# Kernel tuning notes

Measured on AMD Instinct MI355X. Metric: run time of the kernel, lower is better.

Reference implementation:

```python
import jax, jax.numpy as jnp
import numpy as np

N = 100000
E = 1600000
IN_DIM = 256
HID = 128


def setup_inputs() -> dict:
    key = jax.random.key(0)
    k = jax.random.split(key, 8)
    x = jax.random.normal(k[0], (N, IN_DIM), dtype=jnp.float32)
    edge_index = jax.random.randint(k[1], (2, E), 0, N, dtype=jnp.int64 if jax.config.jax_enable_x64 else jnp.int32)
    # GCNConv weight (no bias pre-aggregation; bias added after aggregation, as in PyG)
    W_conv = jax.random.normal(k[2], (IN_DIM, HID), dtype=jnp.float32) / np.sqrt(IN_DIM)
    b_conv = jnp.zeros((HID,), dtype=jnp.float32)
    prelu_a = jnp.full((1,), 0.25, dtype=jnp.float32)  # torch.nn.PReLU default init
    W_lin = jax.random.normal(k[3], (HID, IN_DIM), dtype=jnp.float32) / np.sqrt(HID)
    b_lin = jnp.zeros((IN_DIM,), dtype=jnp.float32)
    return {"x": x, "edge_index": edge_index, "W_conv": W_conv, "b_conv": b_conv,
            "prelu_a": prelu_a, "W_lin": W_lin, "b_lin": b_lin}


def _gcn_conv(x, edge_index, W, b):
    # h = x @ W  ([N, HID])
    h = x @ W
    src, dst = edge_index[0], edge_index[1]
    # add self-loops
    loops = jnp.arange(N, dtype=src.dtype)
    src = jnp.concatenate([src, loops])
    dst = jnp.concatenate([dst, loops])
    # symmetric degree normalization deg^-1/2 (degree over incoming edges incl. self-loops)
    deg = jax.ops.segment_sum(jnp.ones_like(dst, dtype=h.dtype), dst, num_segments=N)
    dinv = jnp.where(deg > 0, jax.lax.rsqrt(deg), 0.0)
    norm = dinv[src] * dinv[dst]                     # [E+N]
    msg = h[src] * norm[:, None]                     # gather + scale  [E+N, HID]
    out = jax.ops.segment_sum(msg, dst, num_segments=N)  # scatter-add  [N, HID]
    return out + b


def reference(x, edge_index, W_conv, b_conv, prelu_a, W_lin, b_lin):
    h = _gcn_conv(x, edge_index, W_conv, b_conv)
    h = jnp.where(h >= 0, h, prelu_a * h)            # PReLU (single shared slope)
    # dropout p=0.0 -> identity
    return h @ W_lin + b_lin                          # [N, IN_DIM]
```

## Files before the change

kernel.cpp:

```cpp
#include <hip/hip_runtime.h>

#define N_NODES 100000
#define E_EDGES 1600000
#define INDIM 256
#define HID 128
#define CAP 48
#define NPART 8
#define PART_SZ 12500
#define ECAP 32768
#define PA_BLOCKS 1563
#define PA_STRIDE (PA_BLOCKS * 256)
#define G1_BLOCKS 1563
#define PB_BLOCKS 1024
#define GG_BLOCKS 3125

typedef __attribute__((ext_vector_type(8))) short s16x8;
typedef __attribute__((ext_vector_type(4))) float f32x4;
typedef __attribute__((ext_vector_type(4))) unsigned int u32x4;

__device__ __forceinline__ unsigned short cvt_bf16(float f) {
    unsigned int u = __float_as_uint(f);
    u += 0x7FFFu + ((u >> 16) & 1u);
    return (unsigned short)(u >> 16);
}
__device__ __forceinline__ float bf16_to_f(unsigned short s) {
    return __uint_as_float(((unsigned int)s) << 16);
}

__global__ __launch_bounds__(256) void parta_kernel(const int* __restrict__ src,
                                                    const int* __restrict__ dst,
                                                    int* __restrict__ gcnt,
                                                    unsigned int* __restrict__ pedges,
                                                    const float* __restrict__ Wc,
                                                    const float* __restrict__ Wl,
                                                    unsigned short* __restrict__ f1,
                                                    unsigned short* __restrict__ f2,
                                                    int* __restrict__ count) {
    __shared__ int sCount[8];
    __shared__ int sBase[8];
    const int tid = threadIdx.x;

    if (blockIdx.x < 256) {
        int pt = blockIdx.x * 256 + tid;
        if (pt < 32768) {
            int j = pt & 7, L = (pt >> 3) & 63, t = (pt >> 9) & 7, c = pt >> 12;
            int k = c * 32 + ((L >> 4) * 8) + j;
            int n = t * 16 + (L & 15);
            f1[pt] = cvt_bf16(Wc[k * 128 + n]);
        } else {
            int u = pt - 32768;
            int j = u & 7, L = (u >> 3) & 63, t = (u >> 9) & 15, c = u >> 13;
            int k = c * 32 + ((L >> 4) * 8) + j;
            int n = t * 16 + (L & 15);
            f2[u] = cvt_bf16(Wl[k * 256 + n]);
        }
    } else if (blockIdx.x < 512) {
        for (int i = (blockIdx.x - 256) * 256 + tid; i < 100000; i += 256 * 256)
            count[i] = 0;
    }

    if (tid < 8) sCount[tid] = 0;
    __syncthreads();
    const int lane = tid & 63;
    const int t0 = blockIdx.x * 256 + tid;
    const int xcd = blockIdx.x & 7;

    unsigned int pk[4];
    int pp[4];
    int lo[4];
#pragma unroll
    for (int r = 0; r < 4; ++r) {
        int e = t0 + r * PA_STRIDE;
        bool valid = e < E_EDGES;
        int d = 0, s = 0;
        if (valid) {
            d = __builtin_nontemporal_load(dst + e);
            s = __builtin_nontemporal_load(src + e);
        }
        int p = valid ? d / PART_SZ : 8;
        unsigned long long mask_p = 0ull;
#pragma unroll
        for (int v = 0; v < 8; ++v) {
            unsigned long long mv = __ballot(p == v);
            if (p == v) mask_p = mv;
        }
        int off = __popcll(mask_p & ((1ull << lane) - 1ull));
        int ldr = (mask_p == 0ull) ? 0 : (__ffsll(mask_p) - 1);
        int wbase = 0;
        if (valid && lane == ldr) wbase = atomicAdd(&sCount[p], __popcll(mask_p));
        wbase = __shfl(wbase, ldr);
        pp[r] = p;
        lo[r] = wbase + off;
        pk[r] = ((unsigned int)(d - p * PART_SZ) << 17) | (unsigned int)s;
    }
    __syncthreads();
    if (tid < 8) sBase[tid] = atomicAdd(&gcnt[xcd * 8 + tid], sCount[tid]);
    __syncthreads();
#pragma unroll
    for (int r = 0; r < 4; ++r) {
        if (pp[r] < 8) {
            int pos = sBase[pp[r]] + lo[r];
            if (pos < ECAP)
                __builtin_nontemporal_store(pk[r],
                    pedges + (size_t)(xcd * 8 + pp[r]) * ECAP + pos);
        }
    }
}

__global__ __launch_bounds__(256) void fat_kernel(const float* __restrict__ x,
                                                  const unsigned short* __restrict__ fragW,
                                                  unsigned short* __restrict__ h,
                                                  const unsigned int* __restrict__ pedges,
                                                  const int* __restrict__ gcnt,
                                                  int* __restrict__ count,
                                                  int* __restrict__ bucket) {
    __shared__ __align__(16) unsigned short xs[64 * 48];
    const int tid = threadIdx.x;

    if (blockIdx.x < G1_BLOCKS) {
        const int r0 = blockIdx.x * 64;
        const int w = tid >> 6, lane = tid & 63;
        const int q = lane >> 4, m = lane & 15;
        const int srow = tid >> 2, skg = tid & 3;

        f32x4 acc[8];
#pragma unroll
        for (int t = 0; t < 8; ++t) acc[t] = (f32x4){0.f, 0.f, 0.f, 0.f};

        const s16x8* fwv = (const s16x8*)fragW;

        for (int c = 0; c < 8; ++c) {
            int gr = r0 + srow;
            f32x4 v0 = (f32x4){0.f, 0.f, 0.f, 0.f}, v1 = v0;
            if (gr < N_NODES) {
                const f32x4* p = (const f32x4*)&x[(size_t)gr * INDIM + c * 32 + skg * 8];
                v0 = __builtin_nontemporal_load(p);
                v1 = __builtin_nontemporal_load(p + 1);
            }
            uint4 pk;
            pk.x = ((unsigned)cvt_bf16(v0.y) << 16) | cvt_bf16(v0.x);
            pk.y = ((unsigned)cvt_bf16(v0.w) << 16) | cvt_bf16(v0.z);
            pk.z = ((unsigned)cvt_bf16(v1.y) << 16) | cvt_bf16(v1.x);
            pk.w = ((unsigned)cvt_bf16(v1.w) << 16) | cvt_bf16(v1.z);
            *(uint4*)&xs[srow * 48 + skg * 8] = pk;
            __syncthreads();

            s16x8 a = *(const s16x8*)&xs[(w * 16 + m) * 48 + q * 8];
#pragma unroll
            for (int t = 0; t < 8; ++t) {
                s16x8 b = fwv[(c * 8 + t) * 64 + lane];
                acc[t] = __builtin_amdgcn_mfma_f32_16x16x32_bf16(a, b, acc[t], 0, 0, 0);
            }
            __syncthreads();
        }

        const int row_base = r0 + w * 16 + q * 4;
#pragma unroll
        for (int t = 0; t < 8; ++t) {
#pragma unroll
            for (int r = 0; r < 4; ++r) {
                int row = row_base + r;
                if (row < N_NODES)
                    __builtin_nontemporal_store(cvt_bf16(acc[t][r]),
                        h + (size_t)row * HID + t * 16 + m);
            }
        }
    } else {
        const int part = blockIdx.x & 7;
        const int bslot = (blockIdx.x - G1_BLOCKS) >> 3;
#pragma unroll
        for (int xx = 0; xx < 8; ++xx) {
            int n = gcnt[xx * 8 + part];
            if (n > ECAP) n = ECAP;
            const unsigned int* lst = pedges + (size_t)(xx * 8 + part) * ECAP;
            for (int i = bslot * 256 + tid; i < n; i += (PB_BLOCKS / 8) * 256) {
                unsigned int v = __builtin_nontemporal_load(lst + i);
                int s = (int)(v & 0x1FFFFu);
                int d = part * PART_SZ + (int)(v >> 17);
                int slot = atomicAdd(&count[d], 1);
                if (slot < CAP) bucket[d * CAP + slot] = s;
            }
        }
    }
}

__device__ __forceinline__ void gather_node(int wid, int lane, int g, int l,
                                            const int* __restrict__ bucket,
                                            const int* __restrict__ count,
                                            const uint4* __restrict__ hp4,
                                            const float* bc, float a,
                                            unsigned int* o) {
    const int raw = count[wid];
    const float dn = rsqrtf((float)(raw + 1));
    int deg = raw > CAP ? CAP : raw;

    int s_l = wid;
    float dv_l = 0.f;
    if (lane < deg) {
        s_l = bucket[wid * CAP + lane];
        dv_l = rsqrtf((float)(count[s_l] + 1));
    }

    float acc[8];
    {
        uint4 hv = hp4[(size_t)wid * 16 + l];
        float w0 = (g == 0) ? dn * dn : 0.f;
        const unsigned int* pv = (const unsigned int*)&hv;
#pragma unroll
        for (int k = 0; k < 4; ++k) {
            acc[2 * k]     = w0 * bf16_to_f((unsigned short)(pv[k] & 0xFFFF));
            acc[2 * k + 1] = w0 * bf16_to_f((unsigned short)(pv[k] >> 16));
        }
    }

    for (int j = 0; j < deg; j += 8) {
        int e0 = j + g;
        int e1 = j + 4 + g;
        int s0 = __shfl(s_l, e0);
        int s1 = __shfl(s_l, e1);
        float w0 = __shfl(dv_l, e0) * dn;
        float w1 = __shfl(dv_l, e1) * dn;
        uint4 hv0 = hp4[(size_t)s0 * 16 + l];
        uint4 hv1 = hp4[(size_t)s1 * 16 + l];
        const unsigned int* p0 = (const unsigned int*)&hv0;
        const unsigned int* p1 = (const unsigned int*)&hv1;
#pragma unroll
        for (int k = 0; k < 4; ++k) {
            acc[2 * k]     += w0 * bf16_to_f((unsigned short)(p0[k] & 0xFFFF));
            acc[2 * k + 1] += w0 * bf16_to_f((unsigned short)(p0[k] >> 16));
        }
#pragma unroll
        for (int k = 0; k < 4; ++k) {
            acc[2 * k]     += w1 * bf16_to_f((unsigned short)(p1[k] & 0xFFFF));
            acc[2 * k + 1] += w1 * bf16_to_f((unsigned short)(p1[k] >> 16));
        }
    }

#pragma unroll
    for (int k = 0; k < 8; ++k) {
        acc[k] += __shfl_xor(acc[k], 16);
        acc[k] += __shfl_xor(acc[k], 32);
    }

#pragma unroll
    for (int k = 0; k < 4; ++k) {
        float ox = acc[2 * k] + bc[2 * k];
        float oy = acc[2 * k + 1] + bc[2 * k + 1];
        ox = ox >= 0.f ? ox : a * ox;
        oy = oy >= 0.f ? oy : a * oy;
        o[k] = ((unsigned)cvt_bf16(oy) << 16) | cvt_bf16(ox);
    }
}

__global__ __launch_bounds__(512) void gg_kernel(const int* __restrict__ bucket,
                                                 const int* __restrict__ count,
                                                 const unsigned short* __restrict__ h,
                                                 const float* __restrict__ b_conv,
                                                 const float* __restrict__ prelu_a,
                                                 const unsigned short* __restrict__ fragW,
                                                 const float* __restrict__ b_lin,
                                                 float* __restrict__ out) {
    __shared__ __align__(16) unsigned short xs[4 * 32 * 48];
    const int tid = threadIdx.x;
    const int wv = tid >> 6;
    const int lane = tid & 63;
    const int g = lane >> 4;
    const int l = lane & 15;
    const int r0 = blockIdx.x * 32;
    const uint4* hp4 = (const uint4*)h;

    const float a = prelu_a[0];
    float bc[8];
    {
        float4 b0 = *(const float4*)&b_conv[l * 8];
        float4 b1 = *(const float4*)&b_conv[l * 8 + 4];
        bc[0] = b0.x; bc[1] = b0.y; bc[2] = b0.z; bc[3] = b0.w;
        bc[4] = b1.x; bc[5] = b1.y; bc[6] = b1.z; bc[7] = b1.w;
    }

#pragma unroll
    for (int k = 0; k < 4; ++k) {
        const int n = wv * 4 + k;
        const int wid = r0 + n;
        unsigned int o[4];
        gather_node(wid, lane, g, l, bucket, count, hp4, bc, a, o);
        if (g == 0) {
            uint4 ov;
            ov.x = o[0]; ov.y = o[1]; ov.z = o[2]; ov.w = o[3];
            *(uint4*)&xs[((l >> 2) * 32 + n) * 48 + (l & 3) * 8] = ov;
        }
    }
    __syncthreads();

    const int q = g, m = l;
    const int rg = wv & 1;
    const int cg = wv >> 1;
    f32x4 acc[4];
#pragma unroll
    for (int t = 0; t < 4; ++t) acc[t] = (f32x4){0.f, 0.f, 0.f, 0.f};

    const s16x8* fwv = (const s16x8*)fragW;
#pragma unroll
    for (int c = 0; c < 4; ++c) {
        s16x8 av = *(const s16x8*)&xs[(c * 32 + rg * 16 + m) * 48 + q * 8];
#pragma unroll
        for (int t = 0; t < 4; ++t) {
            s16x8 b = fwv[(c * 16 + cg * 4 + t) * 64 + lane];
            acc[t] = __builtin_amdgcn_mfma_f32_16x16x32_bf16(av, b, acc[t], 0, 0, 0);
        }
    }

    const int row_base = r0 + rg * 16 + q * 4;
#pragma unroll
    for (int t = 0; t < 4; ++t) {
        int col = (cg * 4 + t) * 16 + m;
        float bias = b_lin[col];
#pragma unroll
        for (int r = 0; r < 4; ++r) {
            int row = row_base + r;
            __builtin_nontemporal_store(acc[t][r] + bias,
                out + (size_t)row * INDIM + col);
        }
    }
}

extern "C" void kernel_launch(void* const* d_in, const int* in_sizes, int n_in,
                              void* d_out, int out_size, void* d_ws, size_t ws_size,
                              hipStream_t stream) {
    const float* x       = (const float*)d_in[0];
    const int*   eidx    = (const int*)d_in[1];
    const float* W_conv  = (const float*)d_in[2];
    const float* b_conv  = (const float*)d_in[3];
    const float* prelu_a = (const float*)d_in[4];
    const float* W_lin   = (const float*)d_in[5];
    const float* b_lin   = (const float*)d_in[6];
    float* out = (float*)d_out;

    const int* src = eidx;
    const int* dst = eidx + E_EDGES;

    char* base = (char*)d_ws;
    const size_t SZ_BUCKET = (size_t)N_NODES * CAP * 4;
    const size_t SZ_H      = (size_t)N_NODES * HID * 2;
    const size_t SZ_PED    = (size_t)64 * ECAP * 4;
    int* bucket = (int*)base;
    unsigned short* h = (unsigned short*)(base + SZ_BUCKET);
    unsigned int* pedges = (unsigned int*)(base + SZ_BUCKET + SZ_H);
    int* count = (int*)(base + SZ_BUCKET + SZ_H + SZ_PED);
    int* gcnt  = count + 100000;
    unsigned short* fragW1 = (unsigned short*)(count + 100352);
    unsigned short* fragW2 = fragW1 + 32768;

    hipMemsetAsync(gcnt, 0, 352 * sizeof(int), stream);

    parta_kernel<<<PA_BLOCKS, 256, 0, stream>>>(src, dst, gcnt, pedges,
                                                W_conv, W_lin, fragW1, fragW2, count);

    fat_kernel<<<G1_BLOCKS + PB_BLOCKS, 256, 0, stream>>>(x, fragW1, h,
                                                          pedges, gcnt, count, bucket);

    gg_kernel<<<GG_BLOCKS, 512, 0, stream>>>(
        bucket, count, h, b_conv, prelu_a, fragW2, b_lin, out);
}
```

Measured before the change: 374.0 us.

## Replace two-pass partitioned edge binning with direct filtered binning fused into GEMM kernel

```diff
diff --git a/kernel.cpp b/kernel.cpp
--- a/kernel.cpp
+++ b/kernel.cpp
@@ -4,14 +4,12 @@
 #define E_EDGES 1600000
 #define INDIM 256
 #define HID 128
-#define CAP 48
+#define CAP 64
 #define NPART 8
 #define PART_SZ 12500
-#define ECAP 32768
-#define PA_BLOCKS 1563
-#define PA_STRIDE (PA_BLOCKS * 256)
+#define BIN_BLOCKS 2048
+#define NCHUNK 256
 #define G1_BLOCKS 1563
-#define PB_BLOCKS 1024
 #define GG_BLOCKS 3125
 
 typedef __attribute__((ext_vector_type(8))) short s16x8;
@@ -27,21 +25,15 @@
     return __uint_as_float(((unsigned int)s) << 16);
 }
 
-__global__ __launch_bounds__(256) void parta_kernel(const int* __restrict__ src,
-                                                    const int* __restrict__ dst,
-                                                    int* __restrict__ gcnt,
-                                                    unsigned int* __restrict__ pedges,
-                                                    const float* __restrict__ Wc,
-                                                    const float* __restrict__ Wl,
-                                                    unsigned short* __restrict__ f1,
-                                                    unsigned short* __restrict__ f2,
-                                                    int* __restrict__ count) {
-    __shared__ int sCount[8];
-    __shared__ int sBase[8];
+__global__ __launch_bounds__(256) void prepzero_kernel(const float* __restrict__ Wc,
+                                                       const float* __restrict__ Wl,
+                                                       unsigned short* __restrict__ f1,
+                                                       unsigned short* __restrict__ f2,
+                                                       int* __restrict__ count) {
+    const int b = blockIdx.x;
     const int tid = threadIdx.x;
-
-    if (blockIdx.x < 256) {
-        int pt = blockIdx.x * 256 + tid;
+    if (b < 256) {
+        int pt = b * 256 + tid;
         if (pt < 32768) {
             int j = pt & 7, L = (pt >> 3) & 63, t = (pt >> 9) & 7, c = pt >> 12;
             int k = c * 32 + ((L >> 4) * 8) + j;
@@ -54,71 +46,36 @@
             int n = t * 16 + (L & 15);
             f2[u] = cvt_bf16(Wl[k * 256 + n]);
         }
-    } else if (blockIdx.x < 512) {
-        for (int i = (blockIdx.x - 256) * 256 + tid; i < 100000; i += 256 * 256)
-            count[i] = 0;
-    }
-
-    if (tid < 8) sCount[tid] = 0;
-    __syncthreads();
-    const int lane = tid & 63;
-    const int t0 = blockIdx.x * 256 + tid;
-    const int xcd = blockIdx.x & 7;
-
-    unsigned int pk[4];
-    int pp[4];
-    int lo[4];
-#pragma unroll
-    for (int r = 0; r < 4; ++r) {
-        int e = t0 + r * PA_STRIDE;
-        bool valid = e < E_EDGES;
-        int d = 0, s = 0;
-        if (valid) {
-            d = __builtin_nontemporal_load(dst + e);
-            s = __builtin_nontemporal_load(src + e);
-        }
-        int p = valid ? d / PART_SZ : 8;
-        unsigned long long mask_p = 0ull;
-#pragma unroll
-        for (int v = 0; v < 8; ++v) {
-            unsigned long long mv = __ballot(p == v);
-            if (p == v) mask_p = mv;
-        }
-        int off = __popcll(mask_p & ((1ull << lane) - 1ull));
-        int ldr = (mask_p == 0ull) ? 0 : (__ffsll(mask_p) - 1);
-        int wbase = 0;
-        if (valid && lane == ldr) wbase = atomicAdd(&sCount[p], __popcll(mask_p));
-        wbase = __shfl(wbase, ldr);
-        pp[r] = p;
-        lo[r] = wbase + off;
-        pk[r] = ((unsigned int)(d - p * PART_SZ) << 17) | (unsigned int)s;
-    }
-    __syncthreads();
-    if (tid < 8) sBase[tid] = atomicAdd(&gcnt[xcd * 8 + tid], sCount[tid]);
-    __syncthreads();
-#pragma unroll
-    for (int r = 0; r < 4; ++r) {
-        if (pp[r] < 8) {
-            int pos = sBase[pp[r]] + lo[r];
-            if (pos < ECAP)
-                __builtin_nontemporal_store(pk[r],
-                    pedges + (size_t)(xcd * 8 + pp[r]) * ECAP + pos);
-        }
-    }
-}
-
-__global__ __launch_bounds__(256) void fat_kernel(const float* __restrict__ x,
-                                                  const unsigned short* __restrict__ fragW,
-                                                  unsigned short* __restrict__ h,
-                                                  const unsigned int* __restrict__ pedges,
-                                                  const int* __restrict__ gcnt,
-                                                  int* __restrict__ count,
-                                                  int* __restrict__ bucket) {
+    } else {
+        for (int i = (b - 256) * 256 + tid; i < 100352; i += 256 * 256) count[i] = 0;
+    }
+}
+
+__global__ __launch_bounds__(256) void fat3_kernel(const int* __restrict__ src,
+                                                   const int* __restrict__ dst,
+                                                   int* __restrict__ count,
+                                                   int* __restrict__ bucket,
+                                                   const float* __restrict__ x,
+                                                   const unsigned short* __restrict__ fragW,
+                                                   unsigned short* __restrict__ h) {
     __shared__ __align__(16) unsigned short xs[64 * 48];
     const int tid = threadIdx.x;
 
-    if (blockIdx.x < G1_BLOCKS) {
-        const int r0 = blockIdx.x * 64;
+    if (blockIdx.x < BIN_BLOCKS) {
+        const int part = blockIdx.x & (NPART - 1);
+        const int chunk = blockIdx.x >> 3;
+        const int lo = part * PART_SZ;
+        const int hi = lo + PART_SZ;
+        for (int e = chunk * 256 + tid; e < E_EDGES; e += NCHUNK * 256) {
+            int d = dst[e];
+            if (d >= lo && d < hi) {
+                int s = src[e];
+                int slot = atomicAdd(&count[d], 1);
+                if (slot < CAP) bucket[d * CAP + slot] = s;
+            }
+        }
+    } else {
+        const int r0 = (blockIdx.x - BIN_BLOCKS) * 64;
         const int w = tid >> 6, lane = tid & 63;
         const int q = lane >> 4, m = lane & 15;
         const int srow = tid >> 2, skg = tid & 3;
@@ -163,22 +120,6 @@
                 if (row < N_NODES)
                     __builtin_nontemporal_store(cvt_bf16(acc[t][r]),
                         h + (size_t)row * HID + t * 16 + m);
-            }
-        }
-    } else {
-        const int part = blockIdx.x & 7;
-        const int bslot = (blockIdx.x - G1_BLOCKS) >> 3;
-#pragma unroll
-        for (int xx = 0; xx < 8; ++xx) {
-            int n = gcnt[xx * 8 + part];
-            if (n > ECAP) n = ECAP;
-            const unsigned int* lst = pedges + (size_t)(xx * 8 + part) * ECAP;
-            for (int i = bslot * 256 + tid; i < n; i += (PB_BLOCKS / 8) * 256) {
-                unsigned int v = __builtin_nontemporal_load(lst + i);
-                int s = (int)(v & 0x1FFFFu);
-                int d = part * PART_SZ + (int)(v >> 17);
-                int slot = atomicAdd(&count[d], 1);
-                if (slot < CAP) bucket[d * CAP + slot] = s;
             }
         }
     }
@@ -342,22 +283,16 @@
     char* base = (char*)d_ws;
     const size_t SZ_BUCKET = (size_t)N_NODES * CAP * 4;
     const size_t SZ_H      = (size_t)N_NODES * HID * 2;
-    const size_t SZ_PED    = (size_t)64 * ECAP * 4;
     int* bucket = (int*)base;
     unsigned short* h = (unsigned short*)(base + SZ_BUCKET);
-    unsigned int* pedges = (unsigned int*)(base + SZ_BUCKET + SZ_H);
-    int* count = (int*)(base + SZ_BUCKET + SZ_H + SZ_PED);
-    int* gcnt  = count + 100000;
+    int* count = (int*)(base + SZ_BUCKET + SZ_H);
     unsigned short* fragW1 = (unsigned short*)(count + 100352);
     unsigned short* fragW2 = fragW1 + 32768;
 
-    hipMemsetAsync(gcnt, 0, 352 * sizeof(int), stream);
-
-    parta_kernel<<<PA_BLOCKS, 256, 0, stream>>>(src, dst, gcnt, pedges,
-                                                W_conv, W_lin, fragW1, fragW2, count);
-
-    fat_kernel<<<G1_BLOCKS + PB_BLOCKS, 256, 0, stream>>>(x, fragW1, h,
-                                                          pedges, gcnt, count, bucket);
+    prepzero_kernel<<<512, 256, 0, stream>>>(W_conv, W_lin, fragW1, fragW2, count);
+
+    fat3_kernel<<<BIN_BLOCKS + G1_BLOCKS, 256, 0, stream>>>(
+        src, dst, count, bucket, x, fragW1, h);
 
     gg_kernel<<<GG_BLOCKS, 512, 0, stream>>>(
         bucket, count, h, b_conv, prelu_a, fragW2, b_lin, out);
```

New measurement: 378.6 us. No clear change (+1.2%).
